# Kernel optimization log

Measured on AMD Instinct MI355X. Metric: run time of the kernel, lower is better.

Reference implementation:

```python
import jax, jax.numpy as jnp
import numpy as np

NUM_HEADS = 8
IN_DIM = 384
HEAD_DIM = IN_DIM // NUM_HEADS  # 48


def setup_inputs() -> dict:
    key = jax.random.key(0)
    ks = jax.random.split(key, 6)
    B, N, M, C = 4, 4096, 1024, 384
    q_x = jax.random.normal(ks[0], (B, N, C), dtype=jnp.float32)
    kv_x = jax.random.normal(ks[1], (B, M, C), dtype=jnp.float32)
    s = C ** -0.5  # fan-in style init scale
    Wq = jax.random.normal(ks[2], (C, IN_DIM), dtype=jnp.float32) * s
    Wkv = jax.random.normal(ks[3], (C, 2 * IN_DIM), dtype=jnp.float32) * s
    Wproj = jax.random.normal(ks[4], (IN_DIM, IN_DIM), dtype=jnp.float32) * (IN_DIM ** -0.5)
    bproj = jnp.zeros((IN_DIM,), dtype=jnp.float32)
    return {"q_x": q_x, "kv_x": kv_x, "Wq": Wq, "Wkv": Wkv, "Wproj": Wproj, "bproj": bproj}


def reference(q_x, kv_x, Wq, Wkv, Wproj, bproj):
    B, N, C = q_x.shape
    M = kv_x.shape[1]
    scale = HEAD_DIM ** -0.5
    # q: [B, H, N, hd]
    q = (q_x @ Wq).reshape(B, N, NUM_HEADS, HEAD_DIM).transpose(0, 2, 1, 3)
    # k, v: [B, H, M, hd]
    kv = (kv_x @ Wkv).reshape(B, M, 2, NUM_HEADS, HEAD_DIM).transpose(2, 0, 3, 1, 4)
    k, v = kv[0], kv[1]
    # attention scores [B, H, N, M]
    attn = jax.nn.softmax(jnp.einsum('bhnd,bhmd->bhnm', q, k) * scale, axis=-1)
    x = jnp.einsum('bhnm,bhmd->bhnd', attn, v)  # [B, H, N, hd]
    x = x.transpose(0, 2, 1, 3).reshape(B, N, IN_DIM)
    x = x @ Wproj + bproj
    # sr_ratio == 1 residual: add raw q projection back
    q_res = q.transpose(0, 2, 1, 3).reshape(B, N, IN_DIM)
    return q_res + x
```

## Files before the change

kernel.cpp:

```cpp
#include <hip/hip_runtime.h>
#include <hip/hip_bf16.h>
#include <math.h>

#define B_ 4
#define N_ 4096
#define M_ 1024
#define C_ 384
#define NH_ 8
#define HD_ 48

typedef float f32x4 __attribute__((ext_vector_type(4)));
typedef short bf16x8 __attribute__((ext_vector_type(8)));

__device__ __forceinline__ unsigned short f2bf(float x) {
    unsigned int u = __builtin_bit_cast(unsigned int, x);
    return (unsigned short)((u + 0x7FFFu + ((u >> 16) & 1u)) >> 16);
}
__device__ __forceinline__ unsigned short f2bf_trunc(float x) {
    return (unsigned short)(__builtin_bit_cast(unsigned int, x) >> 16);
}
__device__ __forceinline__ float bf2f(unsigned short x) {
    return __builtin_bit_cast(float, (unsigned int)x << 16);
}
__device__ __forceinline__ float fast_exp2(float x) {
#if __has_builtin(__builtin_amdgcn_exp2f)
    return __builtin_amdgcn_exp2f(x);
#else
    return exp2f(x);
#endif
}
__device__ __forceinline__ uint2 pack4_rne(float a, float b, float c, float d) {
    uint2 r;
    r.x = (unsigned int)f2bf(a) | ((unsigned int)f2bf(b) << 16);
    r.y = (unsigned int)f2bf(c) | ((unsigned int)f2bf(d) << 16);
    return r;
}

#define QSCALE 0.20823490983597203f

__global__ __launch_bounds__(256)
void conv_act(const float* __restrict__ a, unsigned short* __restrict__ da,
              const float* __restrict__ b, unsigned short* __restrict__ db)
{
    size_t i4 = (size_t)blockIdx.x * 256 + threadIdx.x;
    const float* src; unsigned short* dst;
    if (i4 < 1572864u) { src = a; dst = da; }
    else { src = b; dst = db; i4 -= 1572864u; }
    float4 v = *(const float4*)&src[i4 * 4];
    *(uint2*)&dst[i4 * 4] = pack4_rne(v.x, v.y, v.z, v.w);
}

__global__ __launch_bounds__(256)
void transpose_w3(const float* __restrict__ Wq, const float* __restrict__ Wkv,
                  const float* __restrict__ Wproj,
                  unsigned short* __restrict__ Wq_t, unsigned short* __restrict__ Wkv_t,
                  unsigned short* __restrict__ Wproj_t)
{
    __shared__ unsigned short T[64 * 72];
    const int tid = threadIdx.x;
    int bid = blockIdx.x;
    const float* W; unsigned short* Wt; int N, kt, nt;
    if (bid < 36)       { W = Wq;    Wt = Wq_t;    N = 384; kt = bid / 6;  nt = bid - kt * 6; }
    else if (bid < 108) { bid -= 36;  W = Wkv;   Wt = Wkv_t;   N = 768; kt = bid / 12; nt = bid - kt * 12; }
    else                { bid -= 108; W = Wproj; Wt = Wproj_t; N = 384; kt = bid / 6;  nt = bid - kt * 6; }
    const int k0 = kt * 64, n0 = nt * 64;

    #pragma unroll
    for (int it = 0; it < 4; ++it) {
        int k = it * 16 + (tid >> 4);
        int n4 = (tid & 15) * 4;
        float4 v = *(const float4*)&W[(size_t)(k0 + k) * N + n0 + n4];
        T[(n4 + 0) * 72 + k] = f2bf(v.x);
        T[(n4 + 1) * 72 + k] = f2bf(v.y);
        T[(n4 + 2) * 72 + k] = f2bf(v.z);
        T[(n4 + 3) * 72 + k] = f2bf(v.w);
    }
    __syncthreads();
    #pragma unroll
    for (int i = 0; i < 2; ++i) {
        int s = tid + 256 * i;
        int n = s >> 3, part = s & 7;
        *(uint4*)&Wt[(size_t)(n0 + n) * C_ + k0 + part * 8] = *(const uint4*)&T[n * 72 + part * 8];
    }
}

__global__ __launch_bounds__(256)
void gemm_hyb(const unsigned short* __restrict__ A, const unsigned short* __restrict__ Wt,
              float* __restrict__ out0,
              unsigned short* __restrict__ bf0, unsigned short* __restrict__ bf1,
              const unsigned short* __restrict__ addend, const float* __restrict__ bias,
              int mode)
{
    __shared__ unsigned short Ws[64 * 392];
    const int tid = threadIdx.x;
    const int wave = tid >> 6;
    const int lane = tid & 63;
    const int ln = lane & 15;
    const int quad = lane >> 4;
    const int row0 = blockIdx.x * 128;
    const int col0 = blockIdx.y * 64;

    for (int i = tid; i < 3072; i += 256) {
        int n = i / 48, part = i - n * 48;
        *(uint4*)&Ws[n * 392 + part * 8] = *(const uint4*)&Wt[(size_t)(col0 + n) * C_ + part * 8];
    }
    __syncthreads();

    f32x4 acc[2][4];
    #pragma unroll
    for (int rt = 0; rt < 2; ++rt)
        #pragma unroll
        for (int ct = 0; ct < 4; ++ct) acc[rt][ct] = (f32x4){0.f, 0.f, 0.f, 0.f};

    const unsigned short* arow0 = A + (size_t)(row0 + wave * 32 + ln) * C_;
    const unsigned short* arow1 = arow0 + 16 * C_;

    #pragma unroll
    for (int kc = 0; kc < 12; ++kc) {
        bf16x8 b0 = *(const bf16x8*)(arow0 + kc * 32 + quad * 8);
        bf16x8 b1 = *(const bf16x8*)(arow1 + kc * 32 + quad * 8);
        #pragma unroll
        for (int ct = 0; ct < 4; ++ct) {
            bf16x8 aw = *(const bf16x8*)&Ws[(ct * 16 + ln) * 392 + kc * 32 + quad * 8];
            acc[0][ct] = __builtin_amdgcn_mfma_f32_16x16x32_bf16(aw, b0, acc[0][ct], 0, 0, 0);
            acc[1][ct] = __builtin_amdgcn_mfma_f32_16x16x32_bf16(aw, b1, acc[1][ct], 0, 0, 0);
        }
    }

    #pragma unroll
    for (int rt = 0; rt < 2; ++rt) {
        int grow = row0 + wave * 32 + rt * 16 + ln;
        #pragma unroll
        for (int ct = 0; ct < 4; ++ct) {
            int gcb = col0 + ct * 16 + quad * 4;
            f32x4 v = acc[rt][ct];
            if (mode == 0) {
                *(uint2*)&bf1[(size_t)grow * C_ + gcb] = pack4_rne(v[0], v[1], v[2], v[3]);
                int b = grow >> 12, n = grow & (N_ - 1);
                int h = gcb / HD_, d = gcb - h * HD_;
                *(uint2*)&bf0[(((size_t)(b * NH_ + h) * N_) + n) * HD_ + d] =
                    pack4_rne(v[0] * QSCALE, v[1] * QSCALE, v[2] * QSCALE, v[3] * QSCALE);
            } else if (mode == 1) {
                int b = grow >> 10, m = grow & (M_ - 1);
                if (col0 < C_) {
                    int h = gcb / HD_, d = gcb - h * HD_;
                    *(uint2*)&bf0[(((size_t)(b * NH_ + h) * M_) + m) * HD_ + d] =
                        pack4_rne(v[0], v[1], v[2], v[3]);
                } else {
                    int c2 = gcb - C_;
                    int h = c2 / HD_, d = c2 - h * HD_;
                    size_t base = ((size_t)(b * NH_ + h) * HD_ + d) * M_ + m;
                    #pragma unroll
                    for (int r = 0; r < 4; ++r) bf1[base + (size_t)r * M_] = f2bf(v[r]);
                }
            } else {
                size_t idx = (size_t)grow * C_ + gcb;
                uint2 ad = *(const uint2*)&addend[idx];
                float4 bi = *(const float4*)&bias[gcb];
                float4 o;
                o.x = v[0] + bf2f((unsigned short)(ad.x & 0xFFFF)) + bi.x;
                o.y = v[1] + bf2f((unsigned short)(ad.x >> 16))    + bi.y;
                o.z = v[2] + bf2f((unsigned short)(ad.y & 0xFFFF)) + bi.z;
                o.w = v[3] + bf2f((unsigned short)(ad.y >> 16))    + bi.w;
                *(float4*)&out0[idx] = o;
            }
        }
    }
}

__global__ __launch_bounds__(256, 4)
void attn_mfma(const unsigned short* __restrict__ qbf,
               const unsigned short* __restrict__ kbf,
               const unsigned short* __restrict__ vbf,
               unsigned short* __restrict__ of)
{
    __shared__ unsigned short P[4][32 * 72];

    const int tid = threadIdx.x;
    const int wave = tid >> 6;
    const int lane = tid & 63;
    const int ln = lane & 15;
    const int quad = lane >> 4;
    const int bh = blockIdx.x;
    const int n0w = blockIdx.y * 128 + wave * 32;

    const bf16x8 zero8 = (bf16x8){0, 0, 0, 0, 0, 0, 0, 0};

    bf16x8 qb[2][2];
    #pragma unroll
    for (int qt = 0; qt < 2; ++qt) {
        const unsigned short* qp = qbf + ((size_t)bh * N_ + n0w + qt * 16 + ln) * HD_;
        qb[qt][0] = *(const bf16x8*)(qp + quad * 8);
        qb[qt][1] = *(const bf16x8*)(qp + 32 + quad * 8);
        if (quad >= 2) qb[qt][1] = zero8;
    }

    f32x4 O[3][2];
    #pragma unroll
    for (int ot = 0; ot < 3; ++ot)
        #pragma unroll
        for (int qt = 0; qt < 2; ++qt) O[ot][qt] = (f32x4){0.f, 0.f, 0.f, 0.f};
    float rs[2] = {0.f, 0.f};

    const unsigned short* kb = kbf + (size_t)bh * M_ * HD_;
    const unsigned short* vb = vbf + (size_t)bh * HD_ * M_;
    unsigned short* Pw = &P[wave][0];

    for (int mt = 0; mt < M_ / 64; ++mt) {
        __syncthreads();

        f32x4 S[4][2];
        #pragma unroll
        for (int t = 0; t < 4; ++t)
            #pragma unroll
            for (int qt = 0; qt < 2; ++qt) S[t][qt] = (f32x4){0.f, 0.f, 0.f, 0.f};
        #pragma unroll
        for (int t = 0; t < 4; ++t) {
            const unsigned short* kp = kb + (size_t)(mt * 64 + t * 16 + ln) * HD_;
            bf16x8 k0 = *(const bf16x8*)(kp + quad * 8);
            bf16x8 k1 = *(const bf16x8*)(kp + 32 + quad * 8);
            if (quad >= 2) k1 = zero8;
            #pragma unroll
            for (int qt = 0; qt < 2; ++qt) {
                S[t][qt] = __builtin_amdgcn_mfma_f32_16x16x32_bf16(k0, qb[qt][0], S[t][qt], 0, 0, 0);
                S[t][qt] = __builtin_amdgcn_mfma_f32_16x16x32_bf16(k1, qb[qt][1], S[t][qt], 0, 0, 0);
            }
        }

        #pragma unroll
        for (int qt = 0; qt < 2; ++qt)
            #pragma unroll
            for (int t = 0; t < 4; ++t) {
                float p0 = fast_exp2(S[t][qt][0]);
                float p1 = fast_exp2(S[t][qt][1]);
                float p2 = fast_exp2(S[t][qt][2]);
                float p3 = fast_exp2(S[t][qt][3]);
                rs[qt] += (p0 + p1) + (p2 + p3);
                uint2 pk;
                pk.x = (unsigned int)f2bf_trunc(p0) | ((unsigned int)f2bf_trunc(p1) << 16);
                pk.y = (unsigned int)f2bf_trunc(p2) | ((unsigned int)f2bf_trunc(p3) << 16);
                *(uint2*)&Pw[(qt * 16 + ln) * 72 + t * 16 + quad * 4] = pk;
            }

        bf16x8 va[3][2];
        #pragma unroll
        for (int ot = 0; ot < 3; ++ot) {
            const unsigned short* vp = vb + (size_t)(ot * 16 + ln) * M_ + mt * 64;
            va[ot][0] = *(const bf16x8*)(vp + quad * 8);
            va[ot][1] = *(const bf16x8*)(vp + 32 + quad * 8);
        }

        bf16x8 pb[2][2];
        #pragma unroll
        for (int qt = 0; qt < 2; ++qt) {
            const unsigned short* Pr = &Pw[(qt * 16 + ln) * 72];
            pb[qt][0] = *(const bf16x8*)(Pr + quad * 8);
            pb[qt][1] = *(const bf16x8*)(Pr + 32 + quad * 8);
        }
        #pragma unroll
        for (int ot = 0; ot < 3; ++ot)
            #pragma unroll
            for (int qt = 0; qt < 2; ++qt) {
                O[ot][qt] = __builtin_amdgcn_mfma_f32_16x16x32_bf16(va[ot][0], pb[qt][0], O[ot][qt], 0, 0, 0);
                O[ot][qt] = __builtin_amdgcn_mfma_f32_16x16x32_bf16(va[ot][1], pb[qt][1], O[ot][qt], 0, 0, 0);
            }
    }

    float inv[2];
    #pragma unroll
    for (int qt = 0; qt < 2; ++qt) {
        float x = rs[qt];
        x += __shfl_xor(x, 16);
        x += __shfl_xor(x, 32);
        inv[qt] = 1.0f / x;
    }

    const int b = bh >> 3, h = bh & 7;
    #pragma unroll
    for (int ot = 0; ot < 3; ++ot)
        #pragma unroll
        for (int qt = 0; qt < 2; ++qt) {
            size_t grow = (size_t)b * N_ + n0w + qt * 16 + ln;
            int gcol = h * HD_ + ot * 16 + quad * 4;
            *(uint2*)&of[grow * C_ + gcol] =
                pack4_rne(O[ot][qt][0] * inv[qt], O[ot][qt][1] * inv[qt],
                          O[ot][qt][2] * inv[qt], O[ot][qt][3] * inv[qt]);
        }
}

extern "C" void kernel_launch(void* const* d_in, const int* in_sizes, int n_in,
                              void* d_out, int out_size, void* d_ws, size_t ws_size,
                              hipStream_t stream) {
    const float* q_x   = (const float*)d_in[0];
    const float* kv_x  = (const float*)d_in[1];
    const float* Wq    = (const float*)d_in[2];
    const float* Wkv   = (const float*)d_in[3];
    const float* Wproj = (const float*)d_in[4];
    const float* bproj = (const float*)d_in[5];
    float* out = (float*)d_out;

    unsigned short* qx_bf   = (unsigned short*)d_ws;
    unsigned short* kvx_bf  = qx_bf  + 6291456;
    unsigned short* qbf     = kvx_bf + 1572864;
    unsigned short* kbf     = qbf    + 6291456;
    unsigned short* vbf     = kbf    + 1572864;
    unsigned short* qres    = vbf    + 1572864;
    unsigned short* Wq_t    = qres   + 6291456;
    unsigned short* Wkv_t   = Wq_t   + 147456;
    unsigned short* Wproj_t = Wkv_t  + 294912;
    unsigned short* of      = qx_bf;

    dim3 blk(256);

    conv_act<<<dim3(7680), blk, 0, stream>>>(q_x, qx_bf, kv_x, kvx_bf);
    transpose_w3<<<dim3(144), blk, 0, stream>>>(Wq, Wkv, Wproj, Wq_t, Wkv_t, Wproj_t);

    gemm_hyb<<<dim3(128, 6), blk, 0, stream>>>(
        qx_bf, Wq_t, nullptr, qbf, qres, nullptr, nullptr, 0);

    gemm_hyb<<<dim3(32, 12), blk, 0, stream>>>(
        kvx_bf, Wkv_t, nullptr, kbf, vbf, nullptr, nullptr, 1);

    attn_mfma<<<dim3(32, 32), blk, 0, stream>>>(qbf, kbf, vbf, of);

    gemm_hyb<<<dim3(128, 6), blk, 0, stream>>>(
        of, Wproj_t, out, nullptr, nullptr, qres, bproj, 2);
}
```

Measured before the change: 204.0 us.

## Fuse activation conversion into QKV GEMM, merge launches, shrink attention tiles

Drops the standalone fp32-to-bf16 conversion kernel. The Q and KV projections now read fp32 activations and convert them in registers, and both run in a single merged launch. The attention kernel processes 16 query rows per wave instead of 32, doubling the grid. It double-buffers the P tile in shared memory so the per-iteration __syncthreads can be removed, and raises the occupancy hint. The trade-offs are heavier fp32 reads in the GEMM, which are repeated across column blocks, and lower K/V reuse per wave in attention.

```diff
diff --git a/kernel.cpp b/kernel.cpp
--- a/kernel.cpp
+++ b/kernel.cpp
@@ -35,20 +35,15 @@
     r.y = (unsigned int)f2bf(c) | ((unsigned int)f2bf(d) << 16);
     return r;
 }
+__device__ __forceinline__ bf16x8 cvt8(float4 a, float4 b) {
+    uint2 lo = pack4_rne(a.x, a.y, a.z, a.w);
+    uint2 hi = pack4_rne(b.x, b.y, b.z, b.w);
+    union { uint4 u; bf16x8 v; } c;
+    c.u.x = lo.x; c.u.y = lo.y; c.u.z = hi.x; c.u.w = hi.y;
+    return c.v;
+}
 
 #define QSCALE 0.20823490983597203f
-
-__global__ __launch_bounds__(256)
-void conv_act(const float* __restrict__ a, unsigned short* __restrict__ da,
-              const float* __restrict__ b, unsigned short* __restrict__ db)
-{
-    size_t i4 = (size_t)blockIdx.x * 256 + threadIdx.x;
-    const float* src; unsigned short* dst;
-    if (i4 < 1572864u) { src = a; dst = da; }
-    else { src = b; dst = db; i4 -= 1572864u; }
-    float4 v = *(const float4*)&src[i4 * 4];
-    *(uint2*)&dst[i4 * 4] = pack4_rne(v.x, v.y, v.z, v.w);
-}
 
 __global__ __launch_bounds__(256)
 void transpose_w3(const float* __restrict__ Wq, const float* __restrict__ Wkv,
@@ -85,11 +80,91 @@
 }
 
 __global__ __launch_bounds__(256)
-void gemm_hyb(const unsigned short* __restrict__ A, const unsigned short* __restrict__ Wt,
+void gemm_qkv(const float* __restrict__ qx, const float* __restrict__ kvx,
+              const unsigned short* __restrict__ Wqt, const unsigned short* __restrict__ Wkvt,
+              unsigned short* __restrict__ qbf, unsigned short* __restrict__ qres,
+              unsigned short* __restrict__ kbf, unsigned short* __restrict__ vbf)
+{
+    __shared__ unsigned short Ws[64 * 392];
+    const int tid = threadIdx.x;
+    const int wave = tid >> 6;
+    const int lane = tid & 63;
+    const int ln = lane & 15;
+    const int quad = lane >> 4;
+
+    int bid = blockIdx.x;
+    int mode, row0, col0;
+    const float* A; const unsigned short* Wt;
+    if (bid < 768) { mode = 0; int rb = bid / 6;  col0 = (bid - rb * 6) * 64;  row0 = rb * 128; A = qx;  Wt = Wqt; }
+    else { bid -= 768; mode = 1; int rb = bid / 12; col0 = (bid - rb * 12) * 64; row0 = rb * 128; A = kvx; Wt = Wkvt; }
+
+    for (int i = tid; i < 3072; i += 256) {
+        int n = i / 48, part = i - n * 48;
+        *(uint4*)&Ws[n * 392 + part * 8] = *(const uint4*)&Wt[(size_t)(col0 + n) * C_ + part * 8];
+    }
+    __syncthreads();
+
+    f32x4 acc[2][4];
+    #pragma unroll
+    for (int rt = 0; rt < 2; ++rt)
+        #pragma unroll
+        for (int ct = 0; ct < 4; ++ct) acc[rt][ct] = (f32x4){0.f, 0.f, 0.f, 0.f};
+
+    const float* ar0 = A + (size_t)(row0 + wave * 32 + ln) * C_;
+    const float* ar1 = ar0 + 16 * C_;
+
+    #pragma unroll
+    for (int kc = 0; kc < 12; ++kc) {
+        const int ko = kc * 32 + quad * 8;
+        float4 x0 = *(const float4*)(ar0 + ko);
+        float4 x1 = *(const float4*)(ar0 + ko + 4);
+        float4 y0 = *(const float4*)(ar1 + ko);
+        float4 y1 = *(const float4*)(ar1 + ko + 4);
+        bf16x8 b0 = cvt8(x0, x1);
+        bf16x8 b1 = cvt8(y0, y1);
+        #pragma unroll
+        for (int ct = 0; ct < 4; ++ct) {
+            bf16x8 aw = *(const bf16x8*)&Ws[(ct * 16 + ln) * 392 + kc * 32 + quad * 8];
+            acc[0][ct] = __builtin_amdgcn_mfma_f32_16x16x32_bf16(aw, b0, acc[0][ct], 0, 0, 0);
+            acc[1][ct] = __builtin_amdgcn_mfma_f32_16x16x32_bf16(aw, b1, acc[1][ct], 0, 0, 0);
+        }
+    }
+
+    #pragma unroll
+    for (int rt = 0; rt < 2; ++rt) {
+        int grow = row0 + wave * 32 + rt * 16 + ln;
+        #pragma unroll
+        for (int ct = 0; ct < 4; ++ct) {
+            int gcb = col0 + ct * 16 + quad * 4;
+            f32x4 v = acc[rt][ct];
+            if (mode == 0) {
+                *(uint2*)&qres[(size_t)grow * C_ + gcb] = pack4_rne(v[0], v[1], v[2], v[3]);
+                int b = grow >> 12, n = grow & (N_ - 1);
+                int h = gcb / HD_, d = gcb - h * HD_;
+                *(uint2*)&qbf[(((size_t)(b * NH_ + h) * N_) + n) * HD_ + d] =
+                    pack4_rne(v[0] * QSCALE, v[1] * QSCALE, v[2] * QSCALE, v[3] * QSCALE);
+            } else {
+                int b = grow >> 10, m = grow & (M_ - 1);
+                if (col0 < C_) {
+                    int h = gcb / HD_, d = gcb - h * HD_;
+                    *(uint2*)&kbf[(((size_t)(b * NH_ + h) * M_) + m) * HD_ + d] =
+                        pack4_rne(v[0], v[1], v[2], v[3]);
+                } else {
+                    int c2 = gcb - C_;
+                    int h = c2 / HD_, d = c2 - h * HD_;
+                    size_t base = ((size_t)(b * NH_ + h) * HD_ + d) * M_ + m;
+                    #pragma unroll
+                    for (int r = 0; r < 4; ++r) vbf[base + (size_t)r * M_] = f2bf(v[r]);
+                }
+            }
+        }
+    }
+}
+
+__global__ __launch_bounds__(256)
+void gemm_out(const unsigned short* __restrict__ A, const unsigned short* __restrict__ Wt,
               float* __restrict__ out0,
-              unsigned short* __restrict__ bf0, unsigned short* __restrict__ bf1,
-              const unsigned short* __restrict__ addend, const float* __restrict__ bias,
-              int mode)
+              const unsigned short* __restrict__ addend, const float* __restrict__ bias)
 {
     __shared__ unsigned short Ws[64 * 392];
     const int tid = threadIdx.x;
@@ -112,13 +187,13 @@
         #pragma unroll
         for (int ct = 0; ct < 4; ++ct) acc[rt][ct] = (f32x4){0.f, 0.f, 0.f, 0.f};
 
-    const unsigned short* arow0 = A + (size_t)(row0 + wave * 32 + ln) * C_;
-    const unsigned short* arow1 = arow0 + 16 * C_;
+    const unsigned short* ar0 = A + (size_t)(row0 + wave * 32 + ln) * C_;
+    const unsigned short* ar1 = ar0 + 16 * C_;
 
     #pragma unroll
     for (int kc = 0; kc < 12; ++kc) {
-        bf16x8 b0 = *(const bf16x8*)(arow0 + kc * 32 + quad * 8);
-        bf16x8 b1 = *(const bf16x8*)(arow1 + kc * 32 + quad * 8);
+        bf16x8 b0 = *(const bf16x8*)(ar0 + kc * 32 + quad * 8);
+        bf16x8 b1 = *(const bf16x8*)(ar1 + kc * 32 + quad * 8);
         #pragma unroll
         for (int ct = 0; ct < 4; ++ct) {
             bf16x8 aw = *(const bf16x8*)&Ws[(ct * 16 + ln) * 392 + kc * 32 + quad * 8];
@@ -134,47 +209,26 @@
         for (int ct = 0; ct < 4; ++ct) {
             int gcb = col0 + ct * 16 + quad * 4;
             f32x4 v = acc[rt][ct];
-            if (mode == 0) {
-                *(uint2*)&bf1[(size_t)grow * C_ + gcb] = pack4_rne(v[0], v[1], v[2], v[3]);
-                int b = grow >> 12, n = grow & (N_ - 1);
-                int h = gcb / HD_, d = gcb - h * HD_;
-                *(uint2*)&bf0[(((size_t)(b * NH_ + h) * N_) + n) * HD_ + d] =
-                    pack4_rne(v[0] * QSCALE, v[1] * QSCALE, v[2] * QSCALE, v[3] * QSCALE);
-            } else if (mode == 1) {
-                int b = grow >> 10, m = grow & (M_ - 1);
-                if (col0 < C_) {
-                    int h = gcb / HD_, d = gcb - h * HD_;
-                    *(uint2*)&bf0[(((size_t)(b * NH_ + h) * M_) + m) * HD_ + d] =
-                        pack4_rne(v[0], v[1], v[2], v[3]);
-                } else {
-                    int c2 = gcb - C_;
-                    int h = c2 / HD_, d = c2 - h * HD_;
-                    size_t base = ((size_t)(b * NH_ + h) * HD_ + d) * M_ + m;
-                    #pragma unroll
-                    for (int r = 0; r < 4; ++r) bf1[base + (size_t)r * M_] = f2bf(v[r]);
-                }
-            } else {
-                size_t idx = (size_t)grow * C_ + gcb;
-                uint2 ad = *(const uint2*)&addend[idx];
-                float4 bi = *(const float4*)&bias[gcb];
-                float4 o;
-                o.x = v[0] + bf2f((unsigned short)(ad.x & 0xFFFF)) + bi.x;
-                o.y = v[1] + bf2f((unsigned short)(ad.x >> 16))    + bi.y;
-                o.z = v[2] + bf2f((unsigned short)(ad.y & 0xFFFF)) + bi.z;
-                o.w = v[3] + bf2f((unsigned short)(ad.y >> 16))    + bi.w;
-                *(float4*)&out0[idx] = o;
-            }
-        }
-    }
-}
-
-__global__ __launch_bounds__(256, 4)
+            size_t idx = (size_t)grow * C_ + gcb;
+            uint2 ad = *(const uint2*)&addend[idx];
+            float4 bi = *(const float4*)&bias[gcb];
+            float4 o;
+            o.x = v[0] + bf2f((unsigned short)(ad.x & 0xFFFF)) + bi.x;
+            o.y = v[1] + bf2f((unsigned short)(ad.x >> 16))    + bi.y;
+            o.z = v[2] + bf2f((unsigned short)(ad.y & 0xFFFF)) + bi.z;
+            o.w = v[3] + bf2f((unsigned short)(ad.y >> 16))    + bi.w;
+            *(float4*)&out0[idx] = o;
+        }
+    }
+}
+
+__global__ __launch_bounds__(256, 6)
 void attn_mfma(const unsigned short* __restrict__ qbf,
                const unsigned short* __restrict__ kbf,
                const unsigned short* __restrict__ vbf,
                unsigned short* __restrict__ of)
 {
-    __shared__ unsigned short P[4][32 * 72];
+    __shared__ unsigned short P[4][2][16 * 72];
 
     const int tid = threadIdx.x;
     const int wave = tid >> 6;
@@ -182,65 +236,38 @@
     const int ln = lane & 15;
     const int quad = lane >> 4;
     const int bh = blockIdx.x;
-    const int n0w = blockIdx.y * 128 + wave * 32;
+    const int n0w = blockIdx.y * 64 + wave * 16;
 
     const bf16x8 zero8 = (bf16x8){0, 0, 0, 0, 0, 0, 0, 0};
 
-    bf16x8 qb[2][2];
-    #pragma unroll
-    for (int qt = 0; qt < 2; ++qt) {
-        const unsigned short* qp = qbf + ((size_t)bh * N_ + n0w + qt * 16 + ln) * HD_;
-        qb[qt][0] = *(const bf16x8*)(qp + quad * 8);
-        qb[qt][1] = *(const bf16x8*)(qp + 32 + quad * 8);
-        if (quad >= 2) qb[qt][1] = zero8;
-    }
-
-    f32x4 O[3][2];
-    #pragma unroll
-    for (int ot = 0; ot < 3; ++ot)
-        #pragma unroll
-        for (int qt = 0; qt < 2; ++qt) O[ot][qt] = (f32x4){0.f, 0.f, 0.f, 0.f};
-    float rs[2] = {0.f, 0.f};
+    const unsigned short* qp = qbf + ((size_t)bh * N_ + n0w + ln) * HD_;
+    bf16x8 qb0 = *(const bf16x8*)(qp + quad * 8);
+    bf16x8 qb1 = *(const bf16x8*)(qp + 32 + quad * 8);
+    if (quad >= 2) qb1 = zero8;
+
+    f32x4 O[3];
+    #pragma unroll
+    for (int ot = 0; ot < 3; ++ot) O[ot] = (f32x4){0.f, 0.f, 0.f, 0.f};
+    float rs = 0.f;
 
     const unsigned short* kb = kbf + (size_t)bh * M_ * HD_;
     const unsigned short* vb = vbf + (size_t)bh * HD_ * M_;
-    unsigned short* Pw = &P[wave][0];
 
     for (int mt = 0; mt < M_ / 64; ++mt) {
-        __syncthreads();
-
-        f32x4 S[4][2];
-        #pragma unroll
-        for (int t = 0; t < 4; ++t)
-            #pragma unroll
-            for (int qt = 0; qt < 2; ++qt) S[t][qt] = (f32x4){0.f, 0.f, 0.f, 0.f};
+        unsigned short* Pw = &P[wave][mt & 1][0];
+
+        f32x4 S[4];
+        #pragma unroll
+        for (int t = 0; t < 4; ++t) S[t] = (f32x4){0.f, 0.f, 0.f, 0.f};
         #pragma unroll
         for (int t = 0; t < 4; ++t) {
             const unsigned short* kp = kb + (size_t)(mt * 64 + t * 16 + ln) * HD_;
             bf16x8 k0 = *(const bf16x8*)(kp + quad * 8);
             bf16x8 k1 = *(const bf16x8*)(kp + 32 + quad * 8);
             if (quad >= 2) k1 = zero8;
-            #pragma unroll
-            for (int qt = 0; qt < 2; ++qt) {
-                S[t][qt] = __builtin_amdgcn_mfma_f32_16x16x32_bf16(k0, qb[qt][0], S[t][qt], 0, 0, 0);
-                S[t][qt] = __builtin_amdgcn_mfma_f32_16x16x32_bf16(k1, qb[qt][1], S[t][qt], 0, 0, 0);
-            }
-        }
-
-        #pragma unroll
-        for (int qt = 0; qt < 2; ++qt)
-            #pragma unroll
-            for (int t = 0; t < 4; ++t) {
-                float p0 = fast_exp2(S[t][qt][0]);
-                float p1 = fast_exp2(S[t][qt][1]);
-                float p2 = fast_exp2(S[t][qt][2]);
-                float p3 = fast_exp2(S[t][qt][3]);
-                rs[qt] += (p0 + p1) + (p2 + p3);
-                uint2 pk;
-                pk.x = (unsigned int)f2bf_trunc(p0) | ((unsigned int)f2bf_trunc(p1) << 16);
-                pk.y = (unsigned int)f2bf_trunc(p2) | ((unsigned int)f2bf_trunc(p3) << 16);
-                *(uint2*)&Pw[(qt * 16 + ln) * 72 + t * 16 + quad * 4] = pk;
-            }
+            S[t] = __builtin_amdgcn_mfma_f32_16x16x32_bf16(k0, qb0, S[t], 0, 0, 0);
+            S[t] = __builtin_amdgcn_mfma_f32_16x16x32_bf16(k1, qb1, S[t], 0, 0, 0);
+        }
 
         bf16x8 va[3][2];
         #pragma unroll
@@ -250,42 +277,42 @@
             va[ot][1] = *(const bf16x8*)(vp + 32 + quad * 8);
         }
 
-        bf16x8 pb[2][2];
-        #pragma unroll
-        for (int qt = 0; qt < 2; ++qt) {
-            const unsigned short* Pr = &Pw[(qt * 16 + ln) * 72];
-            pb[qt][0] = *(const bf16x8*)(Pr + quad * 8);
-            pb[qt][1] = *(const bf16x8*)(Pr + 32 + quad * 8);
-        }
-        #pragma unroll
-        for (int ot = 0; ot < 3; ++ot)
-            #pragma unroll
-            for (int qt = 0; qt < 2; ++qt) {
-                O[ot][qt] = __builtin_amdgcn_mfma_f32_16x16x32_bf16(va[ot][0], pb[qt][0], O[ot][qt], 0, 0, 0);
-                O[ot][qt] = __builtin_amdgcn_mfma_f32_16x16x32_bf16(va[ot][1], pb[qt][1], O[ot][qt], 0, 0, 0);
-            }
-    }
-
-    float inv[2];
-    #pragma unroll
-    for (int qt = 0; qt < 2; ++qt) {
-        float x = rs[qt];
-        x += __shfl_xor(x, 16);
-        x += __shfl_xor(x, 32);
-        inv[qt] = 1.0f / x;
-    }
+        #pragma unroll
+        for (int t = 0; t < 4; ++t) {
+            float p0 = fast_exp2(S[t][0]);
+            float p1 = fast_exp2(S[t][1]);
+            float p2 = fast_exp2(S[t][2]);
+            float p3 = fast_exp2(S[t][3]);
+            rs += (p0 + p1) + (p2 + p3);
+            uint2 pk;
+            pk.x = (unsigned int)f2bf_trunc(p0) | ((unsigned int)f2bf_trunc(p1) << 16);
+            pk.y = (unsigned int)f2bf_trunc(p2) | ((unsigned int)f2bf_trunc(p3) << 16);
+            *(uint2*)&Pw[ln * 72 + t * 16 + quad * 4] = pk;
+        }
+
+        const unsigned short* Pr = &Pw[ln * 72];
+        bf16x8 pb0 = *(const bf16x8*)(Pr + quad * 8);
+        bf16x8 pb1 = *(const bf16x8*)(Pr + 32 + quad * 8);
+        #pragma unroll
+        for (int ot = 0; ot < 3; ++ot) {
+            O[ot] = __builtin_amdgcn_mfma_f32_16x16x32_bf16(va[ot][0], pb0, O[ot], 0, 0, 0);
+            O[ot] = __builtin_amdgcn_mfma_f32_16x16x32_bf16(va[ot][1], pb1, O[ot], 0, 0, 0);
+        }
+    }
+
+    float x = rs;
+    x += __shfl_xor(x, 16);
+    x += __shfl_xor(x, 32);
+    const float inv = 1.0f / x;
 
     const int b = bh >> 3, h = bh & 7;
-    #pragma unroll
-    for (int ot = 0; ot < 3; ++ot)
-        #pragma unroll
-        for (int qt = 0; qt < 2; ++qt) {
-            size_t grow = (size_t)b * N_ + n0w + qt * 16 + ln;
-            int gcol = h * HD_ + ot * 16 + quad * 4;
-            *(uint2*)&of[grow * C_ + gcol] =
-                pack4_rne(O[ot][qt][0] * inv[qt], O[ot][qt][1] * inv[qt],
-                          O[ot][qt][2] * inv[qt], O[ot][qt][3] * inv[qt]);
-        }
+    size_t grow = (size_t)b * N_ + n0w + ln;
+    #pragma unroll
+    for (int ot = 0; ot < 3; ++ot) {
+        int gcol = h * HD_ + ot * 16 + quad * 4;
+        *(uint2*)&of[grow * C_ + gcol] =
+            pack4_rne(O[ot][0] * inv, O[ot][1] * inv, O[ot][2] * inv, O[ot][3] * inv);
+    }
 }
 
 extern "C" void kernel_launch(void* const* d_in, const int* in_sizes, int n_in,
@@ -299,30 +326,24 @@
     const float* bproj = (const float*)d_in[5];
     float* out = (float*)d_out;
 
-    unsigned short* qx_bf   = (unsigned short*)d_ws;
-    unsigned short* kvx_bf  = qx_bf  + 6291456;
-    unsigned short* qbf     = kvx_bf + 1572864;
-    unsigned short* kbf     = qbf    + 6291456;
-    unsigned short* vbf     = kbf    + 1572864;
-    unsigned short* qres    = vbf    + 1572864;
-    unsigned short* Wq_t    = qres   + 6291456;
-    unsigned short* Wkv_t   = Wq_t   + 147456;
-    unsigned short* Wproj_t = Wkv_t  + 294912;
-    unsigned short* of      = qx_bf;
+    unsigned short* qbf     = (unsigned short*)d_ws;
+    unsigned short* kbf     = qbf     + 6291456;
+    unsigned short* vbf     = kbf     + 1572864;
+    unsigned short* qres    = vbf     + 1572864;
+    unsigned short* of      = qres    + 6291456;
+    unsigned short* Wq_t    = of      + 6291456;
+    unsigned short* Wkv_t   = Wq_t    + 147456;
+    unsigned short* Wproj_t = Wkv_t   + 294912;
 
     dim3 blk(256);
 
-    conv_act<<<dim3(7680), blk, 0, stream>>>(q_x, qx_bf, kv_x, kvx_bf);
     transpose_w3<<<dim3(144), blk, 0, stream>>>(Wq, Wkv, Wproj, Wq_t, Wkv_t, Wproj_t);
 
-    gemm_hyb<<<dim3(128, 6), blk, 0, stream>>>(
-        qx_bf, Wq_t, nullptr, qbf, qres, nullptr, nullptr, 0);
-
-    gemm_hyb<<<dim3(32, 12), blk, 0, stream>>>(
-        kvx_bf, Wkv_t, nullptr, kbf, vbf, nullptr, nullptr, 1);
-
-    attn_mfma<<<dim3(32, 32), blk, 0, stream>>>(qbf, kbf, vbf, of);
-
-    gemm_hyb<<<dim3(128, 6), blk, 0, stream>>>(
-        of, Wproj_t, out, nullptr, nullptr, qres, bproj, 2);
-}
+    gemm_qkv<<<dim3(1152), blk, 0, stream>>>(
+        q_x, kv_x, Wq_t, Wkv_t, qbf, qres, kbf, vbf);
+
+    attn_mfma<<<dim3(32, 64), blk, 0, stream>>>(qbf, kbf, vbf, of);
+
+    gemm_out<<<dim3(128, 6), blk, 0, stream>>>(
+        of, Wproj_t, out, qres, bproj);
+}
```

Result: slower. 279.7 us (+37.1%).
